# Optimization experiments

Measured on AMD Instinct MI355X. Metric: run time of the kernel, lower is better.

Reference implementation:

```python
import math
import jax, jax.numpy as jnp
import numpy as np

H = 16  # num_heads

def get_alibi_slopes(n):
    def pow2_slopes(n):
        start = 2 ** (-2 ** (-(math.log2(n) - 3)))
        return [start * start ** i for i in range(n)]
    if math.log2(n).is_integer():
        return pow2_slopes(n)
    c = 2 ** math.floor(math.log2(n))
    return pow2_slopes(c) + get_alibi_slopes(2 * c)[0::2][: n - c]

def alibi_bias(num_heads, L, dtype=jnp.float32):
    slopes = jnp.asarray(get_alibi_slopes(num_heads), dtype=dtype)  # [H]
    pos = jnp.arange(L)
    rel = (pos[None, :] - pos[:, None]).astype(dtype)               # [L, L] = x - y
    bias = slopes[:, None, None] * rel[None, :, :]                  # [H, L, L]
    causal = pos[None, :] <= pos[:, None]                           # tril mask
    return jnp.where(causal[None, :, :], bias, -jnp.inf)


def setup_inputs() -> dict:
    key = jax.random.key(0)
    ks = jax.random.split(key, 4)
    D = 1024
    B, L = 2, 2048
    s_in = 1.0 / math.sqrt(D)
    return {
        "x": jax.random.normal(ks[0], (B, L, D), dtype=jnp.float32),
        "w_in": jax.random.normal(ks[1], (D, 3 * D), dtype=jnp.float32) * s_in,
        "b_in": jnp.zeros((3 * D,), dtype=jnp.float32),
        "w_out": jax.random.normal(ks[2], (D, D), dtype=jnp.float32) * s_in,
        "b_out": jnp.zeros((D,), dtype=jnp.float32),
    }


def reference(x, w_in, b_in, w_out, b_out):
    B, L, D = x.shape
    dh = D // H
    qkv = x @ w_in + b_in                                   # [B, L, 3D]
    q, k, v = jnp.split(qkv, 3, axis=-1)
    # [B, L, D] -> [B, H, L, dh]
    def heads(t):
        return t.reshape(B, L, H, dh).transpose(0, 2, 1, 3)
    q, k, v = heads(q), heads(k), heads(v)
    scores = jnp.einsum("bhqd,bhkd->bhqk", q, k) / math.sqrt(dh)
    scores = scores + alibi_bias(H, L, scores.dtype)[None]  # [B, H, L, L]
    attn = jax.nn.softmax(scores, axis=-1)
    out = jnp.einsum("bhqk,bhkd->bhqd", attn, v)            # [B, H, L, dh]
    out = out.transpose(0, 2, 1, 3).reshape(B, L, D)
    return out @ w_out + b_out
```

## Files before the change

kernel.cpp:

```cpp
#include <hip/hip_runtime.h>
#include <stdint.h>
#include <math.h>

#define NH 16
#define DH 64
#define SEQ 2048
#define DMODEL 1024

typedef short short8 __attribute__((ext_vector_type(8)));
typedef short short4v __attribute__((ext_vector_type(4)));
typedef float f32x4 __attribute__((ext_vector_type(4)));
typedef __bf16 bf16x4 __attribute__((ext_vector_type(4)));

__device__ __forceinline__ short f2bf(float f) {
  __bf16 h = (__bf16)f;
  return __builtin_bit_cast(short, h);
}
__device__ __forceinline__ short4v cvt4(f32x4 v) {
  bf16x4 b = __builtin_convertvector(v, bf16x4);
  return __builtin_bit_cast(short4v, b);
}
__device__ __forceinline__ float fast_exp2(float x) {
#if __has_builtin(__builtin_amdgcn_exp2f)
  return __builtin_amdgcn_exp2f(x);
#else
  return exp2f(x);
#endif
}

typedef const __attribute__((address_space(1))) uint32_t* gp_t;
typedef __attribute__((address_space(3))) uint32_t* lp_t;
__device__ __forceinline__ void async16(const short* g, short* l) {
  __builtin_amdgcn_global_load_lds((gp_t)g, (lp_t)l, 16, 0, 0);
}

__device__ __forceinline__ void transpose_tile(const float* __restrict__ in,
                                               short* __restrict__ out, int R, int C,
                                               int t, int tilesX, int tid) {
  __shared__ float tile[32][33];
  const int tx = tid & 31, ty = tid >> 5;
  const int c0 = (t % tilesX) * 32, r0 = (t / tilesX) * 32;
#pragma unroll
  for (int i = 0; i < 4; ++i)
    tile[ty + i * 8][tx] = in[(size_t)(r0 + ty + i * 8) * C + c0 + tx];
  __syncthreads();
#pragma unroll
  for (int i = 0; i < 4; ++i)
    out[(size_t)(c0 + ty + i * 8) * R + r0 + tx] = f2bf(tile[tx][ty + i * 8]);
}

__global__ void k_prep(const float* __restrict__ x, short* __restrict__ xb,
                       const float* __restrict__ w_in, short* __restrict__ w_in_t,
                       const float* __restrict__ w_out, short* __restrict__ w_out_t) {
  const int tid = threadIdx.x;
  const int blk = blockIdx.x;
  if (blk < 4096) {
    const int i = blk * 256 + tid;
    f32x4 v = ((const f32x4*)x)[i];
    ((short4v*)xb)[i] = cvt4(v);
  } else if (blk < 4096 + 3072) {
    transpose_tile(w_in, w_in_t, 1024, 3072, blk - 4096, 96, tid);
  } else {
    transpose_tile(w_out, w_out_t, 1024, 1024, blk - 7168, 32, tid);
  }
}

template <int MODE>
__launch_bounds__(256, 3)
__global__ void k_gemm(const short* __restrict__ A, const short* __restrict__ Bt,
                       const float* __restrict__ bias, float* __restrict__ Cf,
                       short* __restrict__ qo, short* __restrict__ ko,
                       short* __restrict__ vo) {
  constexpr int KD = 1024;
  __shared__ __align__(16) short As[128 * 64];
  __shared__ __align__(16) short Bs[128 * 64];
  const int tid = threadIdx.x;
  const int wave = tid >> 6, lane = tid & 63;
  const int quad = lane >> 4, l16 = lane & 15;
  const int wm = wave >> 1, wn = wave & 1;
  const int tM = blockIdx.y * 128, tN = blockIdx.x * 128;

  const short* pA[4];
  const short* pB[4];
  short* lA[4];
  short* lB[4];
#pragma unroll
  for (int t = 0; t < 4; ++t) {
    const int c = t * 256 + tid;
    const int row = c >> 3, gch = (c & 7) ^ (row & 7);
    pA[t] = A + (size_t)(tM + row) * KD + gch * 8;
    pB[t] = Bt + (size_t)(tN + row) * KD + gch * 8;
    lA[t] = &As[c * 8];
    lB[t] = &Bs[c * 8];
  }

  const int sw = l16 & 7;
  const int col0 = (quad ^ sw) << 3;
  const int col1 = col0 ^ 32;

  f32x4 acc[4][4] = {};

  for (int k0 = 0; k0 < KD; k0 += 64) {
    __syncthreads();
#pragma unroll
    for (int t = 0; t < 4; ++t) {
      async16(pA[t] + k0, lA[t]);
      async16(pB[t] + k0, lB[t]);
    }
    __syncthreads();
#pragma unroll
    for (int kh = 0; kh < 2; ++kh) {
      const int col = kh ? col1 : col0;
      short8 af[4], bfr[4];
#pragma unroll
      for (int i = 0; i < 4; ++i)
        af[i] = *(const short8*)&As[(wm * 64 + i * 16 + l16) * 64 + col];
#pragma unroll
      for (int i = 0; i < 4; ++i)
        bfr[i] = *(const short8*)&Bs[(wn * 64 + i * 16 + l16) * 64 + col];
#pragma unroll
      for (int i = 0; i < 4; ++i)
#pragma unroll
        for (int j = 0; j < 4; ++j)
          acc[i][j] = __builtin_amdgcn_mfma_f32_16x16x32_bf16(af[i], bfr[j], acc[i][j], 0, 0, 0);
    }
  }

  const int rbase = tM + wm * 64 + quad * 4;
#pragma unroll
  for (int i = 0; i < 4; ++i) {
#pragma unroll
    for (int j = 0; j < 4; ++j) {
      const int col = tN + wn * 64 + j * 16 + l16;
      const float bi = bias[col];
      if (MODE == 0) {
        const int which = col >> 10;
        const int h = (col & 1023) >> 6, d = col & 63;
        if (which == 2) {
          const int row0 = rbase + i * 16;
          const int b = row0 >> 11, li0 = row0 & 2047;
          f32x4 t;
#pragma unroll
          for (int rr = 0; rr < 4; ++rr) t[rr] = acc[i][j][rr] + bi;
          *(short4v*)&vo[(((size_t)(b * NH + h)) * DH + d) * SEQ + li0] = cvt4(t);
        } else {
          short* dst = (which == 0) ? qo : ko;
#pragma unroll
          for (int rr = 0; rr < 4; ++rr) {
            const int row = rbase + i * 16 + rr;
            const int b = row >> 11, li = row & 2047;
            dst[(((size_t)(b * NH + h)) * SEQ + li) * DH + d] = f2bf(acc[i][j][rr] + bi);
          }
        }
      } else {
#pragma unroll
        for (int rr = 0; rr < 4; ++rr) {
          const int row = rbase + i * 16 + rr;
          Cf[(size_t)row * DMODEL + col] = acc[i][j][rr] + bi;
        }
      }
    }
  }
}

__launch_bounds__(256)
__global__ void k_attn(const short* __restrict__ q, const short* __restrict__ k,
                       const short* __restrict__ vt, short* __restrict__ o) {
  __shared__ __align__(16) short Ks[2][64 * 64];
  __shared__ __align__(16) short Vs[2][64 * 64];
  __shared__ __align__(16) short Ps[4][16 * 64];
  const int tid = threadIdx.x;
  const int wave = tid >> 6, lane = tid & 63;
  const int quad = lane >> 4, l16 = lane & 15;
  const int sw = l16 & 7;
  const int qt = 31 - (blockIdx.x >> 5);
  const int bh = blockIdx.x & 31;
  const int h = bh & (NH - 1);
  const size_t base = (size_t)bh * SEQ * DH;
  const float LOG2E = 1.44269504088896f;
  const float slope2 = exp2f(-0.5f * (float)(h + 1)) * LOG2E;
  const float scale2 = 0.125f * LOG2E;
  const float FM = 12.0f;

  const int c0i = tid, c1i = 256 + tid;
  const int r0 = c0i >> 3, ch0 = (c0i & 7) ^ (r0 & 7);
  const int r1 = c1i >> 3, ch1 = (c1i & 7) ^ (r1 & 7);
  const int qk_off0 = r0 * DH + ch0 * 8;
  const int qk_off1 = r1 * DH + ch1 * 8;
  const int v_off0 = r0 * SEQ + ch0 * 8;
  const int v_off1 = r1 * SEQ + ch1 * 8;

  const int col0 = ((quad ^ sw) << 3);
  const int col1 = col0 ^ 32;
  int psoff[4];
#pragma unroll
  for (int in = 0; in < 4; ++in)
    psoff[in] = l16 * 64 + (((2 * in + (quad >> 1)) ^ sw) << 3) + (quad & 1) * 4;
  const int qlim4 = wave * 16 + l16 - 4 * quad;

  const int q0 = qt * 64;
  const int qrow = q0 + wave * 16 + l16;
  const short* qp = q + base + (size_t)qrow * DH + quad * 8;
  const short8 qb0 = *(const short8*)qp;
  const short8 qb1 = *(const short8*)(qp + 32);

  short8 ones;
#pragma unroll
  for (int j = 0; j < 8; ++j) ones[j] = (short)0x3F80;

  f32x4 accO[4] = {};
  f32x4 accL = {};
  const float qoff = -slope2 * (float)qrow - FM + slope2 * (float)(4 * quad);
  float inoff[4];
#pragma unroll
  for (int in = 0; in < 4; ++in)
    inoff[in] = qoff + slope2 * (float)(16 * in);
  const float s64 = slope2 * 64.0f;
  float rc[4];
#pragma unroll
  for (int r = 0; r < 4; ++r) rc[r] = slope2 * (float)r;

  const short* kp = k + base;
  const short* vp = vt + base;

  async16(kp + qk_off0, &Ks[0][c0i * 8]);
  async16(kp + qk_off1, &Ks[0][c1i * 8]);
  async16(vp + v_off0, &Vs[0][c0i * 8]);
  async16(vp + v_off1, &Vs[0][c1i * 8]);
  kp += 64 * DH;
  vp += 64;
  __syncthreads();

  for (int kt = 0; kt <= qt; ++kt) {
    const int cur = kt & 1, nxt = cur ^ 1;
    if (kt < qt) {
      async16(kp + qk_off0, &Ks[nxt][c0i * 8]);
      async16(kp + qk_off1, &Ks[nxt][c1i * 8]);
      async16(vp + v_off0, &Vs[nxt][c0i * 8]);
      async16(vp + v_off1, &Vs[nxt][c1i * 8]);
      kp += 64 * DH;
      vp += 64;
    }

    f32x4 s[4];
#pragma unroll
    for (int in = 0; in < 4; ++in) {
      const short8 ka0 = *(const short8*)&Ks[cur][(in * 16 + l16) * 64 + col0];
      const short8 ka1 = *(const short8*)&Ks[cur][(in * 16 + l16) * 64 + col1];
      f32x4 t = {};
      t = __builtin_amdgcn_mfma_f32_16x16x32_bf16(ka0, qb0, t, 0, 0, 0);
      t = __builtin_amdgcn_mfma_f32_16x16x32_bf16(ka1, qb1, t, 0, 0, 0);
      s[in] = t;
    }

    if (kt == qt) {
#pragma unroll
      for (int in = 0; in < 4; ++in) {
        f32x4 p;
#pragma unroll
        for (int r = 0; r < 4; ++r) {
          float val = fast_exp2(fmaf(s[in][r], scale2, inoff[in] + rc[r]));
          p[r] = (16 * in + r <= qlim4) ? val : 0.f;
        }
        *(short4v*)&Ps[wave][psoff[in]] = cvt4(p);
      }
    } else {
#pragma unroll
      for (int in = 0; in < 4; ++in) {
        f32x4 p;
#pragma unroll
        for (int r = 0; r < 4; ++r)
          p[r] = fast_exp2(fmaf(s[in][r], scale2, inoff[in] + rc[r]));
        *(short4v*)&Ps[wave][psoff[in]] = cvt4(p);
      }
    }
#pragma unroll
    for (int in = 0; in < 4; ++in) inoff[in] += s64;

    const short8 pa0 = *(const short8*)&Ps[wave][l16 * 64 + col0];
    const short8 pa1 = *(const short8*)&Ps[wave][l16 * 64 + col1];
    accL = __builtin_amdgcn_mfma_f32_16x16x32_bf16(ones, pa0, accL, 0, 0, 0);
    accL = __builtin_amdgcn_mfma_f32_16x16x32_bf16(ones, pa1, accL, 0, 0, 0);
#pragma unroll
    for (int i = 0; i < 4; ++i) {
      const short8 va0 = *(const short8*)&Vs[cur][(i * 16 + l16) * 64 + col0];
      const short8 va1 = *(const short8*)&Vs[cur][(i * 16 + l16) * 64 + col1];
      accO[i] = __builtin_amdgcn_mfma_f32_16x16x32_bf16(va0, pa0, accO[i], 0, 0, 0);
      accO[i] = __builtin_amdgcn_mfma_f32_16x16x32_bf16(va1, pa1, accO[i], 0, 0, 0);
    }
    __syncthreads();
  }

  const float inv = 1.0f / accL[0];
  const int b = bh >> 4;
  short* ob = o + ((((size_t)b * SEQ + qrow) * NH + h) * DH + 4 * quad);
#pragma unroll
  for (int i = 0; i < 4; ++i) {
    f32x4 t;
#pragma unroll
    for (int r = 0; r < 4; ++r) t[r] = accO[i][r] * inv;
    *(short4v*)&ob[16 * i] = cvt4(t);
  }
}

extern "C" void kernel_launch(void* const* d_in, const int* in_sizes, int n_in,
                              void* d_out, int out_size, void* d_ws, size_t ws_size,
                              hipStream_t stream) {
  const float* x = (const float*)d_in[0];
  const float* w_in = (const float*)d_in[1];
  const float* b_in = (const float*)d_in[2];
  const float* w_out = (const float*)d_in[3];
  const float* b_out = (const float*)d_in[4];
  float* out = (float*)d_out;

  char* ws = (char*)d_ws;
  short* xb = (short*)(ws);
  short* w_in_t = (short*)(ws + (8u << 20));
  short* w_out_t = (short*)(ws + (14u << 20));
  short* qv = (short*)(ws + (16u << 20));
  short* kv = (short*)(ws + (24u << 20));
  short* vv = (short*)(ws + (32u << 20));
  short* ao = (short*)(ws + (40u << 20));

  k_prep<<<8192, 256, 0, stream>>>(x, xb, w_in, w_in_t, w_out, w_out_t);
  k_gemm<0><<<dim3(24, 32), 256, 0, stream>>>(xb, w_in_t, b_in, nullptr, qv, kv, vv);
  k_attn<<<1024, 256, 0, stream>>>(qv, kv, vv, ao);
  k_gemm<1><<<dim3(8, 32), 256, 0, stream>>>(ao, w_out_t, b_out, out, nullptr, nullptr, nullptr);
}
```

Measured before the change: 174.6 us.

## Process two 64-row query tiles per attention block to reuse K/V tiles

Each attention block now handles 128 query rows (two 64-row sub-tiles) and shares every K/V tile loaded into shared memory between both, halving the grid to 512 blocks. The diagonal tile for the second sub-tile is handled in an epilogue after the main loop, and the block order is remapped so heavy and light causal tiles interleave. This cuts K/V global/LDS traffic per query row and adds MFMA work per tile, at the cost of more registers (launch bounds set to 2 blocks per SIMD), a doubled P buffer and fewer blocks in flight.

```diff
diff --git a/kernel.cpp b/kernel.cpp
--- a/kernel.cpp
+++ b/kernel.cpp
@@ -163,17 +163,18 @@
   }
 }
 
-__launch_bounds__(256)
+__launch_bounds__(256, 2)
 __global__ void k_attn(const short* __restrict__ q, const short* __restrict__ k,
                        const short* __restrict__ vt, short* __restrict__ o) {
   __shared__ __align__(16) short Ks[2][64 * 64];
   __shared__ __align__(16) short Vs[2][64 * 64];
-  __shared__ __align__(16) short Ps[4][16 * 64];
+  __shared__ __align__(16) short Ps[2][4][16 * 64];
   const int tid = threadIdx.x;
   const int wave = tid >> 6, lane = tid & 63;
   const int quad = lane >> 4, l16 = lane & 15;
   const int sw = l16 & 7;
-  const int qt = 31 - (blockIdx.x >> 5);
+  const int g = blockIdx.x >> 5;
+  const int qtp = (g < 8) ? (15 - g) : (g - 8);
   const int bh = blockIdx.x & 31;
   const int h = bh & (NH - 1);
   const size_t base = (size_t)bh * SEQ * DH;
@@ -198,24 +199,29 @@
     psoff[in] = l16 * 64 + (((2 * in + (quad >> 1)) ^ sw) << 3) + (quad & 1) * 4;
   const int qlim4 = wave * 16 + l16 - 4 * quad;
 
-  const int q0 = qt * 64;
-  const int qrow = q0 + wave * 16 + l16;
-  const short* qp = q + base + (size_t)qrow * DH + quad * 8;
-  const short8 qb0 = *(const short8*)qp;
-  const short8 qb1 = *(const short8*)(qp + 32);
+  const int q0 = qtp * 128;
+  const int ktmax = 2 * qtp + 1;
+  const int qrow0 = q0 + wave * 16 + l16;
+  const int qrow1 = qrow0 + 64;
+  const short* qp0 = q + base + (size_t)qrow0 * DH + quad * 8;
+  const short* qp1 = q + base + (size_t)qrow1 * DH + quad * 8;
+  const short8 qA0 = *(const short8*)qp0;
+  const short8 qA1 = *(const short8*)(qp0 + 32);
+  const short8 qB0 = *(const short8*)qp1;
+  const short8 qB1 = *(const short8*)(qp1 + 32);
 
   short8 ones;
 #pragma unroll
   for (int j = 0; j < 8; ++j) ones[j] = (short)0x3F80;
 
-  f32x4 accO[4] = {};
-  f32x4 accL = {};
-  const float qoff = -slope2 * (float)qrow - FM + slope2 * (float)(4 * quad);
+  f32x4 accO[2][4] = {};
+  f32x4 accL[2] = {};
+  const float qoff = -slope2 * (float)qrow0 - FM + slope2 * (float)(4 * quad);
+  const float d64 = slope2 * 64.0f;
   float inoff[4];
 #pragma unroll
   for (int in = 0; in < 4; ++in)
     inoff[in] = qoff + slope2 * (float)(16 * in);
-  const float s64 = slope2 * 64.0f;
   float rc[4];
 #pragma unroll
   for (int r = 0; r < 4; ++r) rc[r] = slope2 * (float)r;
@@ -231,38 +237,40 @@
   vp += 64;
   __syncthreads();
 
-  for (int kt = 0; kt <= qt; ++kt) {
+  for (int kt = 0; kt < ktmax; ++kt) {
     const int cur = kt & 1, nxt = cur ^ 1;
-    if (kt < qt) {
-      async16(kp + qk_off0, &Ks[nxt][c0i * 8]);
-      async16(kp + qk_off1, &Ks[nxt][c1i * 8]);
-      async16(vp + v_off0, &Vs[nxt][c0i * 8]);
-      async16(vp + v_off1, &Vs[nxt][c1i * 8]);
-      kp += 64 * DH;
-      vp += 64;
-    }
-
-    f32x4 s[4];
+    async16(kp + qk_off0, &Ks[nxt][c0i * 8]);
+    async16(kp + qk_off1, &Ks[nxt][c1i * 8]);
+    async16(vp + v_off0, &Vs[nxt][c0i * 8]);
+    async16(vp + v_off1, &Vs[nxt][c1i * 8]);
+    kp += 64 * DH;
+    vp += 64;
+
+    f32x4 s0[4], s1[4];
 #pragma unroll
     for (int in = 0; in < 4; ++in) {
       const short8 ka0 = *(const short8*)&Ks[cur][(in * 16 + l16) * 64 + col0];
       const short8 ka1 = *(const short8*)&Ks[cur][(in * 16 + l16) * 64 + col1];
-      f32x4 t = {};
-      t = __builtin_amdgcn_mfma_f32_16x16x32_bf16(ka0, qb0, t, 0, 0, 0);
-      t = __builtin_amdgcn_mfma_f32_16x16x32_bf16(ka1, qb1, t, 0, 0, 0);
-      s[in] = t;
-    }
-
-    if (kt == qt) {
+      f32x4 t0 = {};
+      t0 = __builtin_amdgcn_mfma_f32_16x16x32_bf16(ka0, qA0, t0, 0, 0, 0);
+      t0 = __builtin_amdgcn_mfma_f32_16x16x32_bf16(ka1, qA1, t0, 0, 0, 0);
+      s0[in] = t0;
+      f32x4 t1 = {};
+      t1 = __builtin_amdgcn_mfma_f32_16x16x32_bf16(ka0, qB0, t1, 0, 0, 0);
+      t1 = __builtin_amdgcn_mfma_f32_16x16x32_bf16(ka1, qB1, t1, 0, 0, 0);
+      s1[in] = t1;
+    }
+
+    if (kt == ktmax - 1) {
 #pragma unroll
       for (int in = 0; in < 4; ++in) {
         f32x4 p;
 #pragma unroll
         for (int r = 0; r < 4; ++r) {
-          float val = fast_exp2(fmaf(s[in][r], scale2, inoff[in] + rc[r]));
+          float val = fast_exp2(fmaf(s0[in][r], scale2, inoff[in] + rc[r]));
           p[r] = (16 * in + r <= qlim4) ? val : 0.f;
         }
-        *(short4v*)&Ps[wave][psoff[in]] = cvt4(p);
+        *(short4v*)&Ps[0][wave][psoff[in]] = cvt4(p);
       }
     } else {
 #pragma unroll
@@ -270,36 +278,89 @@
         f32x4 p;
 #pragma unroll
         for (int r = 0; r < 4; ++r)
-          p[r] = fast_exp2(fmaf(s[in][r], scale2, inoff[in] + rc[r]));
-        *(short4v*)&Ps[wave][psoff[in]] = cvt4(p);
+          p[r] = fast_exp2(fmaf(s0[in][r], scale2, inoff[in] + rc[r]));
+        *(short4v*)&Ps[0][wave][psoff[in]] = cvt4(p);
       }
     }
 #pragma unroll
-    for (int in = 0; in < 4; ++in) inoff[in] += s64;
-
-    const short8 pa0 = *(const short8*)&Ps[wave][l16 * 64 + col0];
-    const short8 pa1 = *(const short8*)&Ps[wave][l16 * 64 + col1];
-    accL = __builtin_amdgcn_mfma_f32_16x16x32_bf16(ones, pa0, accL, 0, 0, 0);
-    accL = __builtin_amdgcn_mfma_f32_16x16x32_bf16(ones, pa1, accL, 0, 0, 0);
+    for (int in = 0; in < 4; ++in) {
+      f32x4 p;
+#pragma unroll
+      for (int r = 0; r < 4; ++r)
+        p[r] = fast_exp2(fmaf(s1[in][r], scale2, (inoff[in] - d64) + rc[r]));
+      *(short4v*)&Ps[1][wave][psoff[in]] = cvt4(p);
+    }
+#pragma unroll
+    for (int in = 0; in < 4; ++in) inoff[in] += d64;
+
+    const short8 pa00 = *(const short8*)&Ps[0][wave][l16 * 64 + col0];
+    const short8 pa01 = *(const short8*)&Ps[0][wave][l16 * 64 + col1];
+    const short8 pa10 = *(const short8*)&Ps[1][wave][l16 * 64 + col0];
+    const short8 pa11 = *(const short8*)&Ps[1][wave][l16 * 64 + col1];
+    accL[0] = __builtin_amdgcn_mfma_f32_16x16x32_bf16(ones, pa00, accL[0], 0, 0, 0);
+    accL[0] = __builtin_amdgcn_mfma_f32_16x16x32_bf16(ones, pa01, accL[0], 0, 0, 0);
+    accL[1] = __builtin_amdgcn_mfma_f32_16x16x32_bf16(ones, pa10, accL[1], 0, 0, 0);
+    accL[1] = __builtin_amdgcn_mfma_f32_16x16x32_bf16(ones, pa11, accL[1], 0, 0, 0);
 #pragma unroll
     for (int i = 0; i < 4; ++i) {
       const short8 va0 = *(const short8*)&Vs[cur][(i * 16 + l16) * 64 + col0];
       const short8 va1 = *(const short8*)&Vs[cur][(i * 16 + l16) * 64 + col1];
-      accO[i] = __builtin_amdgcn_mfma_f32_16x16x32_bf16(va0, pa0, accO[i], 0, 0, 0);
-      accO[i] = __builtin_amdgcn_mfma_f32_16x16x32_bf16(va1, pa1, accO[i], 0, 0, 0);
+      accO[0][i] = __builtin_amdgcn_mfma_f32_16x16x32_bf16(va0, pa00, accO[0][i], 0, 0, 0);
+      accO[0][i] = __builtin_amdgcn_mfma_f32_16x16x32_bf16(va1, pa01, accO[0][i], 0, 0, 0);
+      accO[1][i] = __builtin_amdgcn_mfma_f32_16x16x32_bf16(va0, pa10, accO[1][i], 0, 0, 0);
+      accO[1][i] = __builtin_amdgcn_mfma_f32_16x16x32_bf16(va1, pa11, accO[1][i], 0, 0, 0);
     }
     __syncthreads();
   }
 
-  const float inv = 1.0f / accL[0];
+  {
+    const int cur = ktmax & 1;
+    f32x4 s1[4];
+#pragma unroll
+    for (int in = 0; in < 4; ++in) {
+      const short8 ka0 = *(const short8*)&Ks[cur][(in * 16 + l16) * 64 + col0];
+      const short8 ka1 = *(const short8*)&Ks[cur][(in * 16 + l16) * 64 + col1];
+      f32x4 t1 = {};
+      t1 = __builtin_amdgcn_mfma_f32_16x16x32_bf16(ka0, qB0, t1, 0, 0, 0);
+      t1 = __builtin_amdgcn_mfma_f32_16x16x32_bf16(ka1, qB1, t1, 0, 0, 0);
+      s1[in] = t1;
+    }
+#pragma unroll
+    for (int in = 0; in < 4; ++in) {
+      f32x4 p;
+#pragma unroll
+      for (int r = 0; r < 4; ++r) {
+        float val = fast_exp2(fmaf(s1[in][r], scale2, (inoff[in] - d64) + rc[r]));
+        p[r] = (16 * in + r <= qlim4) ? val : 0.f;
+      }
+      *(short4v*)&Ps[1][wave][psoff[in]] = cvt4(p);
+    }
+    const short8 pa10 = *(const short8*)&Ps[1][wave][l16 * 64 + col0];
+    const short8 pa11 = *(const short8*)&Ps[1][wave][l16 * 64 + col1];
+    accL[1] = __builtin_amdgcn_mfma_f32_16x16x32_bf16(ones, pa10, accL[1], 0, 0, 0);
+    accL[1] = __builtin_amdgcn_mfma_f32_16x16x32_bf16(ones, pa11, accL[1], 0, 0, 0);
+#pragma unroll
+    for (int i = 0; i < 4; ++i) {
+      const short8 va0 = *(const short8*)&Vs[cur][(i * 16 + l16) * 64 + col0];
+      const short8 va1 = *(const short8*)&Vs[cur][(i * 16 + l16) * 64 + col1];
+      accO[1][i] = __builtin_amdgcn_mfma_f32_16x16x32_bf16(va0, pa10, accO[1][i], 0, 0, 0);
+      accO[1][i] = __builtin_amdgcn_mfma_f32_16x16x32_bf16(va1, pa11, accO[1][i], 0, 0, 0);
+    }
+  }
+
   const int b = bh >> 4;
-  short* ob = o + ((((size_t)b * SEQ + qrow) * NH + h) * DH + 4 * quad);
-#pragma unroll
-  for (int i = 0; i < 4; ++i) {
-    f32x4 t;
-#pragma unroll
-    for (int r = 0; r < 4; ++r) t[r] = accO[i][r] * inv;
-    *(short4v*)&ob[16 * i] = cvt4(t);
+#pragma unroll
+  for (int cs = 0; cs < 2; ++cs) {
+    const float inv = 1.0f / accL[cs][0];
+    const int qrow = (cs == 0) ? qrow0 : qrow1;
+    short* ob = o + ((((size_t)b * SEQ + qrow) * NH + h) * DH + 4 * quad);
+#pragma unroll
+    for (int i = 0; i < 4; ++i) {
+      f32x4 t;
+#pragma unroll
+      for (int r = 0; r < 4; ++r) t[r] = accO[cs][i][r] * inv;
+      *(short4v*)&ob[16 * i] = cvt4(t);
+    }
   }
 }
 
@@ -324,6 +385,6 @@
 
   k_prep<<<8192, 256, 0, stream>>>(x, xb, w_in, w_in_t, w_out, w_out_t);
   k_gemm<0><<<dim3(24, 32), 256, 0, stream>>>(xb, w_in_t, b_in, nullptr, qv, kv, vv);
-  k_attn<<<1024, 256, 0, stream>>>(qv, kv, vv, ao);
+  k_attn<<<512, 256, 0, stream>>>(qv, kv, vv, ao);
   k_gemm<1><<<dim3(8, 32), 256, 0, stream>>>(ao, w_out_t, b_out, out, nullptr, nullptr, nullptr);
 }
```

Result: no change. 176.9 us (+1.3%).
